# Kernel tuning notes

Hardware: AMD Instinct MI355X
Metric: run time of the kernel (lower is better)

Reference implementation:

```python
import jax, jax.numpy as jnp
import numpy as np

D_MODEL, D_K, D_V = 1024, 64, 64
B, S = 4, 2048

def setup_inputs() -> dict:
    key = jax.random.key(0)
    ks = jax.random.split(key, 9)
    lim = 1.0 / np.sqrt(D_MODEL)
    return {
        "query": jax.random.normal(ks[0], (B, S, D_MODEL), jnp.float32),
        "key":   jax.random.normal(ks[1], (B, S, D_MODEL), jnp.float32),
        "value": jax.random.normal(ks[2], (B, S, D_MODEL), jnp.float32),
        "Wq": jax.random.uniform(ks[3], (D_MODEL, D_K), jnp.float32, -lim, lim),
        "bq": jax.random.uniform(ks[4], (D_K,), jnp.float32, -lim, lim),
        "Wk": jax.random.uniform(ks[5], (D_MODEL, D_K), jnp.float32, -lim, lim),
        "bk": jax.random.uniform(ks[6], (D_K,), jnp.float32, -lim, lim),
        "Wv": jax.random.uniform(ks[7], (D_MODEL, D_V), jnp.float32, -lim, lim),
        "bv": jax.random.uniform(ks[8], (D_V,), jnp.float32, -lim, lim),
    }

def reference(query, key, value, Wq, bq, Wk, bk, Wv, bv):
    # Linear projections: [B,S,d_model] -> [B,S,d_k/d_v]
    q = jnp.einsum("bsd,dk->bsk", query, Wq) + bq
    k = jnp.einsum("bsd,dk->bsk", key, Wk) + bk
    v = jnp.einsum("bsd,dv->bsv", value, Wv) + bv
    scale = 1.0 / jnp.sqrt(jnp.asarray(q.shape[-1], q.dtype))
    scores = jnp.einsum("bqk,bsk->bqs", q, k) * scale  # [B,S,S]
    attn = jax.nn.softmax(scores, axis=-1)
    return jnp.einsum("bqs,bsv->bqv", attn, v)  # [B,S,d_v]
```

## Files before the change

kernel.cpp:

```cpp
#include <hip/hip_runtime.h>
#include <hip/hip_bf16.h>


typedef __attribute__((ext_vector_type(8))) short bf16x8;
typedef __attribute__((ext_vector_type(4))) float f32x4;

#define MFMA16(a, b, c) __builtin_amdgcn_mfma_f32_16x16x32_bf16((a), (b), (c), 0, 0, 0)

__device__ __forceinline__ unsigned short f2bf(float x) {
    unsigned int u = __float_as_uint(x);
    u = (u + 0x7FFFu + ((u >> 16) & 1u)) >> 16;
    return (unsigned short)u;
}
__device__ __forceinline__ int pk2(float a, float b) {
    return (int)f2bf(a) | ((int)f2bf(b) << 16);
}

__global__ __launch_bounds__(256) void prep_w(
    const float* __restrict__ Wq, const float* __restrict__ Wk,
    const float* __restrict__ Wv, unsigned short* __restrict__ Wt) {
    int idx = blockIdx.x * 256 + threadIdx.x;
    int t = idx >> 16;
    int r = idx & 0xFFFF;
    int n = r >> 10, kk = r & 1023;
    const float* W = (t == 0) ? Wq : ((t == 1) ? Wk : Wv);
    Wt[idx] = f2bf(W[kk * 64 + n]);
}

__global__ __launch_bounds__(128) void proj_kernel(
    const float* __restrict__ xq, const float* __restrict__ xk,
    const float* __restrict__ xv, const unsigned short* __restrict__ Wt,
    const float* __restrict__ bq, const float* __restrict__ bk,
    const float* __restrict__ bv, unsigned short* __restrict__ outq,
    unsigned short* __restrict__ outk, unsigned short* __restrict__ outvt) {
    const int chunk = blockIdx.x;
    const int t = chunk >> 8;
    const int rb = chunk & 255;
    const float* __restrict__ x = (t == 0) ? xq : ((t == 1) ? xk : xv);
    const float* __restrict__ bias = (t == 0) ? bq : ((t == 1) ? bk : bv);
    const unsigned short* __restrict__ Wtt = Wt + t * 65536;

    const int w = threadIdx.x >> 6, l = threadIdx.x & 63;
    const int lo = l & 15, q4 = l >> 4;
    const int row0 = rb * 32 + w * 16;

    __shared__ __align__(16) unsigned short plv[2][16][24];

    const float* xb = x + (size_t)(row0 + lo) * 1024 + q4 * 8;
    const unsigned short* wb = Wtt + (size_t)lo * 1024 + q4 * 8;

    f32x4 acc[4];
#pragma unroll
    for (int ci = 0; ci < 4; ci++)
        for (int i = 0; i < 4; i++) acc[ci][i] = 0.f;

    for (int ks = 0; ks < 32; ++ks) {
        const int k0 = ks * 32;
        float4 xa = *(const float4*)(xb + k0);
        float4 xc = *(const float4*)(xb + k0 + 4);
        int4 bi;
        bi.x = pk2(xa.x, xa.y);
        bi.y = pk2(xa.z, xa.w);
        bi.z = pk2(xc.x, xc.y);
        bi.w = pk2(xc.z, xc.w);
        bf16x8 bfrag = *(bf16x8*)&bi;
#pragma unroll
        for (int ci = 0; ci < 4; ++ci) {
            bf16x8 afrag = *(const bf16x8*)(wb + ci * 16384 + k0);
            acc[ci] = MFMA16(afrag, bfrag, acc[ci]);
        }
    }

    const float SCQ = 0.125f * 1.44269504088896340736f;
#pragma unroll
    for (int ci = 0; ci < 4; ++ci) {
        const float4 bb = *(const float4*)&bias[ci * 16 + q4 * 4];
        acc[ci][0] += bb.x;
        acc[ci][1] += bb.y;
        acc[ci][2] += bb.z;
        acc[ci][3] += bb.w;
        if (t == 0)
#pragma unroll
            for (int i = 0; i < 4; i++) acc[ci][i] *= SCQ;
    }

    if (t < 2) {
        unsigned short* out = (t == 0) ? outq : outk;
#pragma unroll
        for (int ci = 0; ci < 4; ++ci) {
            ushort4 h;
            h.x = f2bf(acc[ci][0]);
            h.y = f2bf(acc[ci][1]);
            h.z = f2bf(acc[ci][2]);
            h.w = f2bf(acc[ci][3]);
            *(ushort4*)&out[(size_t)(row0 + lo) * 64 + ci * 16 + q4 * 4] = h;
        }
    } else {
        const int b = row0 >> 11;
        const int sl = row0 & 2047;
#pragma unroll
        for (int ci = 0; ci < 4; ++ci) {
#pragma unroll
            for (int i = 0; i < 4; i++)
                plv[w][q4 * 4 + i][lo] = f2bf(acc[ci][i]);
            ushort4 hh = *(ushort4*)&plv[w][l & 15][(l >> 4) * 4];
            *(ushort4*)&outvt[(size_t)(b * 64 + ci * 16 + (l & 15)) * 2048 +
                              sl + (l >> 4) * 4] = hh;
        }
    }
}

__global__ __launch_bounds__(256) void flash_kernel(
    const unsigned short* __restrict__ q, const unsigned short* __restrict__ k,
    const unsigned short* __restrict__ vt, float* __restrict__ Opart,
    float* __restrict__ lpart) {
    const int bx = blockIdx.x;
    const int xcd = bx & 7;
    const int b = xcd >> 1;
    const int j = ((bx >> 3) << 1) | (xcd & 1);
    const int ks = j & 3;
    const int qb = j >> 2;
    const int w = threadIdx.x >> 6, l = threadIdx.x & 63;
    const int lo = l & 15, q4 = l >> 4;

    __shared__ __align__(16) unsigned short pl[4][16][72];

    const int srow = qb * 64 + w * 16;

    const unsigned short* qp = q + (size_t)(b * 2048 + srow + lo) * 64 + q4 * 8;
    bf16x8 aq0 = *(const bf16x8*)(qp);
    bf16x8 aq1 = *(const bf16x8*)(qp + 32);

    f32x4 O[4];
    for (int i = 0; i < 4; i++)
        for (int j2 = 0; j2 < 4; j2++) O[i][j2] = 0.f;
    float ll[4] = {0.f, 0.f, 0.f, 0.f};

    for (int kt = 0; kt < 8; ++kt) {
        const int kb = ks * 512 + kt * 64;
        f32x4 S[4];
        for (int i = 0; i < 4; i++)
            for (int j2 = 0; j2 < 4; j2++) S[i][j2] = 0.f;
        const unsigned short* kp = k + (size_t)(b * 2048 + kb + lo) * 64 + q4 * 8;
#pragma unroll
        for (int ct = 0; ct < 4; ++ct) {
            bf16x8 b0 = *(const bf16x8*)(kp + ct * 1024);
            bf16x8 b1 = *(const bf16x8*)(kp + ct * 1024 + 32);
            S[ct] = MFMA16(aq0, b0, S[ct]);
            S[ct] = MFMA16(aq1, b1, S[ct]);
        }
#pragma unroll
        for (int i = 0; i < 4; i++) {
#pragma unroll
            for (int ct = 0; ct < 4; ++ct) {
                float p = exp2f(S[ct][i]);
                S[ct][i] = p;
                ll[i] += p;
            }
#pragma unroll
            for (int ct = 0; ct < 4; ++ct)
                pl[w][q4 * 4 + i][ct * 16 + lo] = f2bf(S[ct][i]);
        }
        bf16x8 ap0 = *(const bf16x8*)&pl[w][lo][q4 * 8];
        bf16x8 ap1 = *(const bf16x8*)&pl[w][lo][32 + q4 * 8];
        const unsigned short* vp =
            vt + (size_t)(b * 64 + lo) * 2048 + kb + q4 * 8;
#pragma unroll
        for (int ct = 0; ct < 4; ++ct) {
            bf16x8 v0 = *(const bf16x8*)(vp + (size_t)ct * 16 * 2048);
            bf16x8 v1 = *(const bf16x8*)(vp + (size_t)ct * 16 * 2048 + 32);
            O[ct] = MFMA16(ap0, v0, O[ct]);
            O[ct] = MFMA16(ap1, v1, O[ct]);
        }
    }
    float* op = Opart + ((size_t)(b * 4 + ks) * 2048 + srow) * 64;
#pragma unroll
    for (int ct = 0; ct < 4; ++ct)
#pragma unroll
        for (int i = 0; i < 4; i++)
            op[(size_t)(q4 * 4 + i) * 64 + ct * 16 + lo] = O[ct][i];
#pragma unroll
    for (int i = 0; i < 4; i++) {
        float s = ll[i];
        s += __shfl_xor(s, 1);
        s += __shfl_xor(s, 2);
        s += __shfl_xor(s, 4);
        s += __shfl_xor(s, 8);
        if (lo == 0)
            lpart[(size_t)(b * 4 + ks) * 2048 + srow + q4 * 4 + i] = s;
    }
}

__global__ __launch_bounds__(256) void combine_kernel(
    const float* __restrict__ Opart, const float* __restrict__ lpart,
    float* __restrict__ out) {
    int idx = blockIdx.x * 256 + threadIdx.x;
    int rowi = idx >> 4;
    int v4 = (idx & 15) * 4;
    int b = rowi >> 11, s = rowi & 2047;
    float L = 0.f;
#pragma unroll
    for (int ks = 0; ks < 4; ++ks)
        L += lpart[(size_t)(b * 4 + ks) * 2048 + s];
    float inv = 1.f / L;
    float ax = 0.f, ay = 0.f, az = 0.f, aw = 0.f;
#pragma unroll
    for (int ks = 0; ks < 4; ++ks) {
        const float4 o =
            *(const float4*)&Opart[((size_t)(b * 4 + ks) * 2048 + s) * 64 + v4];
        ax += o.x;
        ay += o.y;
        az += o.z;
        aw += o.w;
    }
    float4 res = make_float4(ax * inv, ay * inv, az * inv, aw * inv);
    *(float4*)&out[(size_t)rowi * 64 + v4] = res;
}

extern "C" void kernel_launch(void* const* d_in, const int* in_sizes, int n_in,
                              void* d_out, int out_size, void* d_ws,
                              size_t ws_size, hipStream_t stream) {
    const float* xq = (const float*)d_in[0];
    const float* xk = (const float*)d_in[1];
    const float* xv = (const float*)d_in[2];
    const float* Wq = (const float*)d_in[3];
    const float* bq = (const float*)d_in[4];
    const float* Wk = (const float*)d_in[5];
    const float* bk = (const float*)d_in[6];
    const float* Wv = (const float*)d_in[7];
    const float* bv = (const float*)d_in[8];
    float* out = (float*)d_out;

    char* ws = (char*)d_ws;
    unsigned short* qb = (unsigned short*)(ws);
    unsigned short* kb = (unsigned short*)(ws + (1u << 20));
    unsigned short* vtb = (unsigned short*)(ws + (2u << 20));
    unsigned short* Wt = (unsigned short*)(ws + (3u << 20));
    float* Opart = (float*)(ws + 3538944);
    float* lpart = (float*)(ws + 11927552);

    hipLaunchKernelGGL(prep_w, dim3(768), dim3(256), 0, stream, Wq, Wk, Wv, Wt);
    hipLaunchKernelGGL(proj_kernel, dim3(768), dim3(128), 0, stream, xq, xk, xv,
                       Wt, bq, bk, bv, qb, kb, vtb);
    hipLaunchKernelGGL(flash_kernel, dim3(512), dim3(256), 0, stream, qb, kb,
                       vtb, Opart, lpart);
    hipLaunchKernelGGL(combine_kernel, dim3(512), dim3(256), 0, stream, Opart,
                       lpart, out);
}
```

Measured before the change: 186.8 us.

## Split projection K-dimension across four waves with LDS reduction and register prefetch

The projection kernel now gives each block 16 rows and splits the 1024-long reduction across four waves (256 each). Partial sums are reduced through shared memory, and the kernel launches with double the blocks and four times the waves. Each wave's loop is fully unrolled, and the next step's x and W fragments are prefetched into registers so loads overlap with MFMA. The goal is more memory-level parallelism and occupancy for this bandwidth-bound stage, at the cost of an LDS reduction and a barrier.

```diff
diff --git a/kernel.cpp b/kernel.cpp
--- a/kernel.cpp
+++ b/kernel.cpp
@@ -27,86 +27,101 @@
     Wt[idx] = f2bf(W[kk * 64 + n]);
 }
 
-__global__ __launch_bounds__(128) void proj_kernel(
+__global__ __launch_bounds__(256, 6) void proj_kernel(
     const float* __restrict__ xq, const float* __restrict__ xk,
     const float* __restrict__ xv, const unsigned short* __restrict__ Wt,
     const float* __restrict__ bq, const float* __restrict__ bk,
     const float* __restrict__ bv, unsigned short* __restrict__ outq,
     unsigned short* __restrict__ outk, unsigned short* __restrict__ outvt) {
-    const int chunk = blockIdx.x;
-    const int t = chunk >> 8;
-    const int rb = chunk & 255;
+    const int bx = blockIdx.x;
+    const int t = bx >> 9;
+    const int g = bx & 511;
+    const int row0 = g * 16;
     const float* __restrict__ x = (t == 0) ? xq : ((t == 1) ? xk : xv);
     const float* __restrict__ bias = (t == 0) ? bq : ((t == 1) ? bk : bv);
     const unsigned short* __restrict__ Wtt = Wt + t * 65536;
 
     const int w = threadIdx.x >> 6, l = threadIdx.x & 63;
     const int lo = l & 15, q4 = l >> 4;
-    const int row0 = rb * 32 + w * 16;
-
-    __shared__ __align__(16) unsigned short plv[2][16][24];
-
-    const float* xb = x + (size_t)(row0 + lo) * 1024 + q4 * 8;
-    const unsigned short* wb = Wtt + (size_t)lo * 1024 + q4 * 8;
+    const int kw = w * 256;
+
+    __shared__ float red[4][64][17];
+
+    const float* xb = x + (size_t)(row0 + lo) * 1024 + kw + q4 * 8;
+    const unsigned short* wb = Wtt + (size_t)lo * 1024 + kw + q4 * 8;
 
     f32x4 acc[4];
 #pragma unroll
     for (int ci = 0; ci < 4; ci++)
         for (int i = 0; i < 4; i++) acc[ci][i] = 0.f;
 
-    for (int ks = 0; ks < 32; ++ks) {
-        const int k0 = ks * 32;
-        float4 xa = *(const float4*)(xb + k0);
-        float4 xc = *(const float4*)(xb + k0 + 4);
+    float4 px0 = *(const float4*)(xb);
+    float4 px1 = *(const float4*)(xb + 4);
+    bf16x8 aw[4];
+#pragma unroll
+    for (int ci = 0; ci < 4; ci++) aw[ci] = *(const bf16x8*)(wb + ci * 16384);
+
+#pragma unroll
+    for (int ks = 0; ks < 8; ++ks) {
+        float4 nx0, nx1;
+        bf16x8 nw[4];
+        if (ks < 7) {
+            const float* xn = xb + (ks + 1) * 32;
+            nx0 = *(const float4*)(xn);
+            nx1 = *(const float4*)(xn + 4);
+#pragma unroll
+            for (int ci = 0; ci < 4; ci++)
+                nw[ci] = *(const bf16x8*)(wb + ci * 16384 + (ks + 1) * 32);
+        }
         int4 bi;
-        bi.x = pk2(xa.x, xa.y);
-        bi.y = pk2(xa.z, xa.w);
-        bi.z = pk2(xc.x, xc.y);
-        bi.w = pk2(xc.z, xc.w);
+        bi.x = pk2(px0.x, px0.y);
+        bi.y = pk2(px0.z, px0.w);
+        bi.z = pk2(px1.x, px1.y);
+        bi.w = pk2(px1.z, px1.w);
         bf16x8 bfrag = *(bf16x8*)&bi;
 #pragma unroll
-        for (int ci = 0; ci < 4; ++ci) {
-            bf16x8 afrag = *(const bf16x8*)(wb + ci * 16384 + k0);
-            acc[ci] = MFMA16(afrag, bfrag, acc[ci]);
-        }
-    }
-
+        for (int ci = 0; ci < 4; ++ci) acc[ci] = MFMA16(aw[ci], bfrag, acc[ci]);
+        if (ks < 7) {
+            px0 = nx0;
+            px1 = nx1;
+#pragma unroll
+            for (int ci = 0; ci < 4; ci++) aw[ci] = nw[ci];
+        }
+    }
+
+#pragma unroll
+    for (int ci = 0; ci < 4; ++ci)
+#pragma unroll
+        for (int i = 0; i < 4; i++)
+            red[w][ci * 16 + q4 * 4 + i][lo] = acc[ci][i];
+    __syncthreads();
+
+    const int tid = threadIdx.x;
     const float SCQ = 0.125f * 1.44269504088896340736f;
-#pragma unroll
-    for (int ci = 0; ci < 4; ++ci) {
-        const float4 bb = *(const float4*)&bias[ci * 16 + q4 * 4];
-        acc[ci][0] += bb.x;
-        acc[ci][1] += bb.y;
-        acc[ci][2] += bb.z;
-        acc[ci][3] += bb.w;
-        if (t == 0)
-#pragma unroll
-            for (int i = 0; i < 4; i++) acc[ci][i] *= SCQ;
-    }
-
     if (t < 2) {
+        const int sr = tid >> 4, od4 = (tid & 15) * 4;
+        float s0 = red[0][od4][sr] + red[1][od4][sr] + red[2][od4][sr] + red[3][od4][sr];
+        float s1 = red[0][od4 + 1][sr] + red[1][od4 + 1][sr] + red[2][od4 + 1][sr] + red[3][od4 + 1][sr];
+        float s2 = red[0][od4 + 2][sr] + red[1][od4 + 2][sr] + red[2][od4 + 2][sr] + red[3][od4 + 2][sr];
+        float s3 = red[0][od4 + 3][sr] + red[1][od4 + 3][sr] + red[2][od4 + 3][sr] + red[3][od4 + 3][sr];
+        const float4 bb = *(const float4*)&bias[od4];
+        s0 += bb.x; s1 += bb.y; s2 += bb.z; s3 += bb.w;
+        if (t == 0) { s0 *= SCQ; s1 *= SCQ; s2 *= SCQ; s3 *= SCQ; }
+        ushort4 h;
+        h.x = f2bf(s0); h.y = f2bf(s1); h.z = f2bf(s2); h.w = f2bf(s3);
         unsigned short* out = (t == 0) ? outq : outk;
-#pragma unroll
-        for (int ci = 0; ci < 4; ++ci) {
-            ushort4 h;
-            h.x = f2bf(acc[ci][0]);
-            h.y = f2bf(acc[ci][1]);
-            h.z = f2bf(acc[ci][2]);
-            h.w = f2bf(acc[ci][3]);
-            *(ushort4*)&out[(size_t)(row0 + lo) * 64 + ci * 16 + q4 * 4] = h;
-        }
+        *(ushort4*)&out[(size_t)(row0 + sr) * 64 + od4] = h;
     } else {
-        const int b = row0 >> 11;
-        const int sl = row0 & 2047;
-#pragma unroll
-        for (int ci = 0; ci < 4; ++ci) {
-#pragma unroll
-            for (int i = 0; i < 4; i++)
-                plv[w][q4 * 4 + i][lo] = f2bf(acc[ci][i]);
-            ushort4 hh = *(ushort4*)&plv[w][l & 15][(l >> 4) * 4];
-            *(ushort4*)&outvt[(size_t)(b * 64 + ci * 16 + (l & 15)) * 2048 +
-                              sl + (l >> 4) * 4] = hh;
-        }
+        const int od = tid >> 2, sr4 = (tid & 3) * 4;
+        const int b = row0 >> 11, sl = row0 & 2047;
+        const float bb = bias[od];
+        float s0 = red[0][od][sr4] + red[1][od][sr4] + red[2][od][sr4] + red[3][od][sr4] + bb;
+        float s1 = red[0][od][sr4 + 1] + red[1][od][sr4 + 1] + red[2][od][sr4 + 1] + red[3][od][sr4 + 1] + bb;
+        float s2 = red[0][od][sr4 + 2] + red[1][od][sr4 + 2] + red[2][od][sr4 + 2] + red[3][od][sr4 + 2] + bb;
+        float s3 = red[0][od][sr4 + 3] + red[1][od][sr4 + 3] + red[2][od][sr4 + 3] + red[3][od][sr4 + 3] + bb;
+        ushort4 h;
+        h.x = f2bf(s0); h.y = f2bf(s1); h.z = f2bf(s2); h.w = f2bf(s3);
+        *(ushort4*)&outvt[(size_t)(b * 64 + od) * 2048 + sl + sr4] = h;
     }
 }
 
@@ -240,7 +255,7 @@
     float* lpart = (float*)(ws + 11927552);
 
     hipLaunchKernelGGL(prep_w, dim3(768), dim3(256), 0, stream, Wq, Wk, Wv, Wt);
-    hipLaunchKernelGGL(proj_kernel, dim3(768), dim3(128), 0, stream, xq, xk, xv,
+    hipLaunchKernelGGL(proj_kernel, dim3(1536), dim3(256), 0, stream, xq, xk, xv,
                        Wt, bq, bk, bv, qb, kb, vtb);
     hipLaunchKernelGGL(flash_kernel, dim3(512), dim3(256), 0, stream, qb, kb,
                        vtb, Opart, lpart);
```

Result: slower. 191.6 us (+2.6%).

## Stage projection input rows in LDS and split output columns across waves

Applied to the files above, without the earlier changes.

The projection kernel now loads a 16-row tile of fp32 activations cooperatively with wide loads, converts it to bf16 once, and stores it in shared memory. Each of the four waves then computes one 16-column slice of the 64 outputs, reading B fragments from LDS and prefetching the next weight fragment from global memory. The launch grows to 1536 blocks of 256 threads to raise parallelism and memory-level concurrency for this bandwidth-bound stage. The cost is 33KB of LDS per block, which limits occupancy, plus a barrier.

```diff
diff --git a/kernel.cpp b/kernel.cpp
--- a/kernel.cpp
+++ b/kernel.cpp
@@ -27,86 +27,86 @@
     Wt[idx] = f2bf(W[kk * 64 + n]);
 }
 
-__global__ __launch_bounds__(128) void proj_kernel(
+__global__ __launch_bounds__(256, 4) void proj_kernel(
     const float* __restrict__ xq, const float* __restrict__ xk,
     const float* __restrict__ xv, const unsigned short* __restrict__ Wt,
     const float* __restrict__ bq, const float* __restrict__ bk,
     const float* __restrict__ bv, unsigned short* __restrict__ outq,
     unsigned short* __restrict__ outk, unsigned short* __restrict__ outvt) {
-    const int chunk = blockIdx.x;
-    const int t = chunk >> 8;
-    const int rb = chunk & 255;
+    const int bx = blockIdx.x;
+    const int t = bx >> 9;
+    const int g = bx & 511;
+    const int row0 = g * 16;
     const float* __restrict__ x = (t == 0) ? xq : ((t == 1) ? xk : xv);
     const float* __restrict__ bias = (t == 0) ? bq : ((t == 1) ? bk : bv);
     const unsigned short* __restrict__ Wtt = Wt + t * 65536;
 
-    const int w = threadIdx.x >> 6, l = threadIdx.x & 63;
+    __shared__ __align__(16) unsigned short xl[16][1032];
+    __shared__ __align__(16) unsigned short plv[4][16][20];
+
+    const int tid = threadIdx.x;
+    const int w = tid >> 6, l = tid & 63;
     const int lo = l & 15, q4 = l >> 4;
-    const int row0 = rb * 32 + w * 16;
-
-    __shared__ __align__(16) unsigned short plv[2][16][24];
-
-    const float* xb = x + (size_t)(row0 + lo) * 1024 + q4 * 8;
-    const unsigned short* wb = Wtt + (size_t)lo * 1024 + q4 * 8;
-
-    f32x4 acc[4];
-#pragma unroll
-    for (int ci = 0; ci < 4; ci++)
-        for (int i = 0; i < 4; i++) acc[ci][i] = 0.f;
-
+
+    {
+        const int r = tid >> 4;
+        const int c = (tid & 15) * 8;
+        const float* xr = x + (size_t)(row0 + r) * 1024 + c;
+        float4 fa[8], fb[8];
+#pragma unroll
+        for (int i = 0; i < 8; ++i) {
+            fa[i] = *(const float4*)(xr + i * 128);
+            fb[i] = *(const float4*)(xr + i * 128 + 4);
+        }
+#pragma unroll
+        for (int i = 0; i < 8; ++i) {
+            int4 d;
+            d.x = pk2(fa[i].x, fa[i].y);
+            d.y = pk2(fa[i].z, fa[i].w);
+            d.z = pk2(fb[i].x, fb[i].y);
+            d.w = pk2(fb[i].z, fb[i].w);
+            *(int4*)&xl[r][i * 128 + c] = d;
+        }
+    }
+    __syncthreads();
+
+    const int colw = w * 16;
+    const unsigned short* wbase = Wtt + (size_t)(colw + lo) * 1024 + q4 * 8;
+
+    f32x4 acc;
+    for (int i = 0; i < 4; i++) acc[i] = 0.f;
+
+    bf16x8 afr = *(const bf16x8*)(wbase);
+#pragma unroll
     for (int ks = 0; ks < 32; ++ks) {
-        const int k0 = ks * 32;
-        float4 xa = *(const float4*)(xb + k0);
-        float4 xc = *(const float4*)(xb + k0 + 4);
-        int4 bi;
-        bi.x = pk2(xa.x, xa.y);
-        bi.y = pk2(xa.z, xa.w);
-        bi.z = pk2(xc.x, xc.y);
-        bi.w = pk2(xc.z, xc.w);
-        bf16x8 bfrag = *(bf16x8*)&bi;
-#pragma unroll
-        for (int ci = 0; ci < 4; ++ci) {
-            bf16x8 afrag = *(const bf16x8*)(wb + ci * 16384 + k0);
-            acc[ci] = MFMA16(afrag, bfrag, acc[ci]);
-        }
-    }
-
-    const float SCQ = 0.125f * 1.44269504088896340736f;
-#pragma unroll
-    for (int ci = 0; ci < 4; ++ci) {
-        const float4 bb = *(const float4*)&bias[ci * 16 + q4 * 4];
-        acc[ci][0] += bb.x;
-        acc[ci][1] += bb.y;
-        acc[ci][2] += bb.z;
-        acc[ci][3] += bb.w;
-        if (t == 0)
-#pragma unroll
-            for (int i = 0; i < 4; i++) acc[ci][i] *= SCQ;
+        bf16x8 anx = afr;
+        if (ks < 31) anx = *(const bf16x8*)(wbase + (ks + 1) * 32);
+        bf16x8 bfr = *(const bf16x8*)&xl[lo][ks * 32 + q4 * 8];
+        acc = MFMA16(afr, bfr, acc);
+        afr = anx;
+    }
+
+    const float4 bb = *(const float4*)&bias[colw + q4 * 4];
+    acc[0] += bb.x; acc[1] += bb.y; acc[2] += bb.z; acc[3] += bb.w;
+    if (t == 0) {
+        const float SCQ = 0.125f * 1.44269504088896340736f;
+#pragma unroll
+        for (int i = 0; i < 4; i++) acc[i] *= SCQ;
     }
 
     if (t < 2) {
         unsigned short* out = (t == 0) ? outq : outk;
-#pragma unroll
-        for (int ci = 0; ci < 4; ++ci) {
-            ushort4 h;
-            h.x = f2bf(acc[ci][0]);
-            h.y = f2bf(acc[ci][1]);
-            h.z = f2bf(acc[ci][2]);
-            h.w = f2bf(acc[ci][3]);
-            *(ushort4*)&out[(size_t)(row0 + lo) * 64 + ci * 16 + q4 * 4] = h;
-        }
+        ushort4 h;
+        h.x = f2bf(acc[0]); h.y = f2bf(acc[1]);
+        h.z = f2bf(acc[2]); h.w = f2bf(acc[3]);
+        *(ushort4*)&out[(size_t)(row0 + lo) * 64 + colw + q4 * 4] = h;
     } else {
-        const int b = row0 >> 11;
-        const int sl = row0 & 2047;
-#pragma unroll
-        for (int ci = 0; ci < 4; ++ci) {
-#pragma unroll
-            for (int i = 0; i < 4; i++)
-                plv[w][q4 * 4 + i][lo] = f2bf(acc[ci][i]);
-            ushort4 hh = *(ushort4*)&plv[w][l & 15][(l >> 4) * 4];
-            *(ushort4*)&outvt[(size_t)(b * 64 + ci * 16 + (l & 15)) * 2048 +
-                              sl + (l >> 4) * 4] = hh;
-        }
+        const int b = row0 >> 11, sl = row0 & 2047;
+#pragma unroll
+        for (int i = 0; i < 4; i++)
+            plv[w][q4 * 4 + i][lo] = f2bf(acc[i]);
+        ushort4 hh = *(ushort4*)&plv[w][lo][q4 * 4];
+        *(ushort4*)&outvt[(size_t)(b * 64 + colw + lo) * 2048 + sl + q4 * 4] = hh;
     }
 }
 
@@ -240,7 +240,7 @@
     float* lpart = (float*)(ws + 11927552);
 
     hipLaunchKernelGGL(prep_w, dim3(768), dim3(256), 0, stream, Wq, Wk, Wv, Wt);
-    hipLaunchKernelGGL(proj_kernel, dim3(768), dim3(128), 0, stream, xq, xk, xv,
+    hipLaunchKernelGGL(proj_kernel, dim3(1536), dim3(256), 0, stream, xq, xk, xv,
                        Wt, bq, bk, bv, qb, kb, vtb);
     hipLaunchKernelGGL(flash_kernel, dim3(512), dim3(256), 0, stream, qb, kb,
                        vtb, Opart, lpart);
```

After: 193.4 us. +3.5%, slower.

## Stage projection inputs and weights through LDS with async double-buffered loads

Applied to the files above, without the earlier changes.

The projection kernel now uses 256 threads per block and copies x rows and a re-laid-out bf16 weight chunk into double-buffered LDS with global_load_lds. The next K-chunk is prefetched while the MFMA loop runs on the current one. Each wave now computes a 16x32 output tile instead of 16x64. The goal is to hide global-load latency and make the weight reads coalesced. The cost is about 133KB of LDS per block, which limits occupancy to one block per CU.

```diff
diff --git a/kernel.cpp b/kernel.cpp
--- a/kernel.cpp
+++ b/kernel.cpp
@@ -16,65 +16,100 @@
     return (int)f2bf(a) | ((int)f2bf(b) << 16);
 }
 
+__device__ __forceinline__ void gll16(const void* g, void* l) {
+    __builtin_amdgcn_global_load_lds(
+        (__attribute__((address_space(1))) void*)(unsigned long long)g,
+        (__attribute__((address_space(3))) void*)(unsigned int)(unsigned long long)l,
+        16, 0, 0);
+}
+
 __global__ __launch_bounds__(256) void prep_w(
     const float* __restrict__ Wq, const float* __restrict__ Wk,
-    const float* __restrict__ Wv, unsigned short* __restrict__ Wt) {
+    const float* __restrict__ Wv, unsigned short* __restrict__ WtS) {
     int idx = blockIdx.x * 256 + threadIdx.x;
     int t = idx >> 16;
     int r = idx & 0xFFFF;
-    int n = r >> 10, kk = r & 1023;
+    int n = r >> 10, k = r & 1023;
+    int kc = k >> 8, k2 = k & 255;
     const float* W = (t == 0) ? Wq : ((t == 1) ? Wk : Wv);
-    Wt[idx] = f2bf(W[kk * 64 + n]);
-}
-
-__global__ __launch_bounds__(128) void proj_kernel(
+    WtS[((size_t)(t * 4 + kc) * 64 + n) * 256 + k2] = f2bf(W[k * 64 + n]);
+}
+
+__global__ __launch_bounds__(256, 1) void proj_kernel(
     const float* __restrict__ xq, const float* __restrict__ xk,
-    const float* __restrict__ xv, const unsigned short* __restrict__ Wt,
+    const float* __restrict__ xv, const unsigned short* __restrict__ WtS,
     const float* __restrict__ bq, const float* __restrict__ bk,
     const float* __restrict__ bv, unsigned short* __restrict__ outq,
     unsigned short* __restrict__ outk, unsigned short* __restrict__ outvt) {
-    const int chunk = blockIdx.x;
-    const int t = chunk >> 8;
-    const int rb = chunk & 255;
+    const int bx = blockIdx.x;
+    const int t = bx >> 8;
+    const int g = bx & 255;
+    const int row0 = g * 32;
     const float* __restrict__ x = (t == 0) ? xq : ((t == 1) ? xk : xv);
     const float* __restrict__ bias = (t == 0) ? bq : ((t == 1) ? bk : bv);
-    const unsigned short* __restrict__ Wtt = Wt + t * 65536;
+
+    __shared__ __align__(16) unsigned char xbuf[2][33280];
+    __shared__ __align__(16) unsigned char wbuf[2][33280];
+    __shared__ __align__(16) unsigned short plv[4][16][20];
 
     const int w = threadIdx.x >> 6, l = threadIdx.x & 63;
     const int lo = l & 15, q4 = l >> 4;
-    const int row0 = rb * 32 + w * 16;
-
-    __shared__ __align__(16) unsigned short plv[2][16][24];
-
-    const float* xb = x + (size_t)(row0 + lo) * 1024 + q4 * 8;
-    const unsigned short* wb = Wtt + (size_t)lo * 1024 + q4 * 8;
-
-    f32x4 acc[4];
-#pragma unroll
-    for (int ci = 0; ci < 4; ci++)
+    const int rowt = (w & 1) * 16;
+    const int colb = (w >> 1) * 32;
+
+    f32x4 acc[2];
+#pragma unroll
+    for (int ci = 0; ci < 2; ci++)
         for (int i = 0; i < 4; i++) acc[ci][i] = 0.f;
 
-    for (int ks = 0; ks < 32; ++ks) {
-        const int k0 = ks * 32;
-        float4 xa = *(const float4*)(xb + k0);
-        float4 xc = *(const float4*)(xb + k0 + 4);
-        int4 bi;
-        bi.x = pk2(xa.x, xa.y);
-        bi.y = pk2(xa.z, xa.w);
-        bi.z = pk2(xc.x, xc.y);
-        bi.w = pk2(xc.z, xc.w);
-        bf16x8 bfrag = *(bf16x8*)&bi;
-#pragma unroll
-        for (int ci = 0; ci < 4; ++ci) {
-            bf16x8 afrag = *(const bf16x8*)(wb + ci * 16384 + k0);
-            acc[ci] = MFMA16(afrag, bfrag, acc[ci]);
-        }
-    }
-
+    auto stage = [&](int kc, int pb) {
+        const float* xg = x + (size_t)(row0 + w * 8) * 1024 + kc * 256 + l * 4;
+        unsigned char* xd = &xbuf[pb][(w * 8) * 1040];
+#pragma unroll
+        for (int i = 0; i < 8; ++i) gll16(xg + i * 1024, xd + i * 1040);
+        const unsigned short* wg =
+            WtS + ((size_t)(t * 4 + kc) * 64 + w * 16) * 256 + l * 8;
+        unsigned char* wd = &wbuf[pb][(w * 8) * 1040];
+#pragma unroll
+        for (int i = 0; i < 8; ++i) gll16(wg + i * 512, wd + i * 1040);
+    };
+
+    auto compute = [&](int pb) {
+        const unsigned char* xs = &xbuf[pb][(rowt + lo) * 1040 + q4 * 32];
+        const unsigned char* wsA = &wbuf[pb][0];
+#pragma unroll
+        for (int step = 0; step < 8; ++step) {
+            float4 b0 = *(const float4*)(xs + step * 128);
+            float4 b1 = *(const float4*)(xs + step * 128 + 16);
+            int4 bi;
+            bi.x = pk2(b0.x, b0.y);
+            bi.y = pk2(b0.z, b0.w);
+            bi.z = pk2(b1.x, b1.y);
+            bi.w = pk2(b1.z, b1.w);
+            bf16x8 bf = *(bf16x8*)&bi;
+#pragma unroll
+            for (int ci = 0; ci < 2; ++ci) {
+                const int n = colb + ci * 16 + lo;
+                bf16x8 af = *(const bf16x8*)(wsA + (n >> 1) * 1040 +
+                                             (n & 1) * 512 + step * 64 + q4 * 16);
+                acc[ci] = MFMA16(af, bf, acc[ci]);
+            }
+        }
+    };
+
+    stage(0, 0);
+    __syncthreads();
+    for (int kc = 0; kc < 4; ++kc) {
+        if (kc < 3) stage(kc + 1, (kc + 1) & 1);
+        compute(kc & 1);
+        __syncthreads();
+    }
+
+    const int seqr = row0 + rowt;
     const float SCQ = 0.125f * 1.44269504088896340736f;
 #pragma unroll
-    for (int ci = 0; ci < 4; ++ci) {
-        const float4 bb = *(const float4*)&bias[ci * 16 + q4 * 4];
+    for (int ci = 0; ci < 2; ++ci) {
+        const float4 bb = *(const float4*)&bias[colb + ci * 16 + q4 * 4];
         acc[ci][0] += bb.x;
         acc[ci][1] += bb.y;
         acc[ci][2] += bb.z;
@@ -83,29 +118,27 @@
 #pragma unroll
             for (int i = 0; i < 4; i++) acc[ci][i] *= SCQ;
     }
-
     if (t < 2) {
         unsigned short* out = (t == 0) ? outq : outk;
 #pragma unroll
-        for (int ci = 0; ci < 4; ++ci) {
+        for (int ci = 0; ci < 2; ++ci) {
             ushort4 h;
             h.x = f2bf(acc[ci][0]);
             h.y = f2bf(acc[ci][1]);
             h.z = f2bf(acc[ci][2]);
             h.w = f2bf(acc[ci][3]);
-            *(ushort4*)&out[(size_t)(row0 + lo) * 64 + ci * 16 + q4 * 4] = h;
+            *(ushort4*)&out[(size_t)(seqr + lo) * 64 + colb + ci * 16 + q4 * 4] = h;
         }
     } else {
-        const int b = row0 >> 11;
-        const int sl = row0 & 2047;
-#pragma unroll
-        for (int ci = 0; ci < 4; ++ci) {
+        const int b = seqr >> 11, sl = seqr & 2047;
+#pragma unroll
+        for (int ci = 0; ci < 2; ++ci) {
 #pragma unroll
             for (int i = 0; i < 4; i++)
                 plv[w][q4 * 4 + i][lo] = f2bf(acc[ci][i]);
-            ushort4 hh = *(ushort4*)&plv[w][l & 15][(l >> 4) * 4];
-            *(ushort4*)&outvt[(size_t)(b * 64 + ci * 16 + (l & 15)) * 2048 +
-                              sl + (l >> 4) * 4] = hh;
+            ushort4 h = *(ushort4*)&plv[w][lo][q4 * 4];
+            *(ushort4*)&outvt[(size_t)(b * 64 + colb + ci * 16 + lo) * 2048 +
+                              sl + q4 * 4] = h;
         }
     }
 }
@@ -235,13 +268,13 @@
     unsigned short* qb = (unsigned short*)(ws);
     unsigned short* kb = (unsigned short*)(ws + (1u << 20));
     unsigned short* vtb = (unsigned short*)(ws + (2u << 20));
-    unsigned short* Wt = (unsigned short*)(ws + (3u << 20));
+    unsigned short* WtS = (unsigned short*)(ws + (3u << 20));
     float* Opart = (float*)(ws + 3538944);
     float* lpart = (float*)(ws + 11927552);
 
-    hipLaunchKernelGGL(prep_w, dim3(768), dim3(256), 0, stream, Wq, Wk, Wv, Wt);
-    hipLaunchKernelGGL(proj_kernel, dim3(768), dim3(128), 0, stream, xq, xk, xv,
-                       Wt, bq, bk, bv, qb, kb, vtb);
+    hipLaunchKernelGGL(prep_w, dim3(768), dim3(256), 0, stream, Wq, Wk, Wv, WtS);
+    hipLaunchKernelGGL(proj_kernel, dim3(768), dim3(256), 0, stream, xq, xk, xv,
+                       WtS, bq, bk, bv, qb, kb, vtb);
     hipLaunchKernelGGL(flash_kernel, dim3(512), dim3(256), 0, stream, qb, kb,
                        vtb, Opart, lpart);
     hipLaunchKernelGGL(combine_kernel, dim3(512), dim3(256), 0, stream, Opart,
```

Result: faster. 180.1 us (-3.6%).
